# Kernel optimization log

Measured on AMD Instinct MI355X. Metric: run time of the kernel, lower is better.

Reference implementation:

```python
import jax, jax.numpy as jnp
import numpy as np

B, T, D, HS = 4, 4096, 1024, 64


def setup_inputs() -> dict:
    key = jax.random.key(0)
    k1, k2, k3 = jax.random.split(key, 3)
    x = jax.random.normal(k1, (B, T, D), dtype=jnp.float32)
    # Linear(n_embd, head_size, bias=False) weights: [head_size, n_embd]
    Wk = jax.random.normal(k2, (HS, D), dtype=jnp.float32) * (D ** -0.5)
    Wv = jax.random.normal(k3, (HS, D), dtype=jnp.float32) * (D ** -0.5)
    return {"x": x, "Wk": Wk, "Wv": Wv}


def reference(x, Wk, Wv):
    # Faithful to source: q = self.value(x) (query proj is dead code), so q and v
    # share the value projection.
    k = jnp.einsum('btd,hd->bth', x, Wk)   # [B,T,HS]
    qv = jnp.einsum('btd,hd->bth', x, Wv)  # [B,T,HS]; serves as both q and v
    scale = k.shape[-1] ** -0.5
    scores = jnp.einsum('bth,bsh->bts', qv, k) * scale  # [B,T,T]
    causal = jnp.tril(jnp.ones((T, T), dtype=bool))
    scores = jnp.where(causal, scores, -jnp.inf)
    weights = jax.nn.softmax(scores, axis=-1)
    out = jnp.einsum('bts,bsh->bth', weights, qv)  # [B,T,HS]
    return out
```

## Files before the change

### kernel.cpp

```cpp
#include <hip/hip_runtime.h>
#include <hip/hip_bf16.h>

typedef __bf16 bf16;
typedef __attribute__((ext_vector_type(4))) __bf16 bf16x4;
typedef __attribute__((ext_vector_type(8))) __bf16 bf16x8;
typedef __attribute__((ext_vector_type(4))) float f32x4;

#define T_SEQ 4096
#define D_EMB 1024
#define HS 64

__device__ __forceinline__ float fexp2(float x) {
#if __has_builtin(__builtin_amdgcn_exp2f)
    return __builtin_amdgcn_exp2f(x);
#else
    return exp2f(x);
#endif
}

__global__ __launch_bounds__(256) void wcast_kernel(
    const float* __restrict__ Wk, const float* __restrict__ Wv,
    bf16* __restrict__ wbf)
{
    const int t = blockIdx.x * 256 + threadIdx.x;
    const int base = t * 8;
    const float* src = (base < 65536) ? (Wk + base) : (Wv + base - 65536);
    float4 f0 = *(const float4*)(src);
    float4 f1 = *(const float4*)(src + 4);
    bf16x8 o = {(__bf16)f0.x, (__bf16)f0.y, (__bf16)f0.z, (__bf16)f0.w,
                (__bf16)f1.x, (__bf16)f1.y, (__bf16)f1.z, (__bf16)f1.w};
    *(bf16x8*)(wbf + base) = o;
}

__global__ __launch_bounds__(256, 2) void proj_kernel(
    const float* __restrict__ x,
    const bf16* __restrict__ wbf,
    bf16* __restrict__ kmat,
    bf16* __restrict__ qvmat,
    bf16* __restrict__ qvT)
{
    __shared__ bf16 xs[2][64][72];
    __shared__ bf16 ws[2][128][72];

    const int tid  = threadIdx.x;
    const int lane = tid & 63;
    const int wave = tid >> 6;
    const int col  = lane & 15;
    const int quad = lane >> 4;
    const int rowbase = blockIdx.x * 64;

    f32x4 acc[4][2];
#pragma unroll
    for (int mt = 0; mt < 4; ++mt)
#pragma unroll
        for (int nt = 0; nt < 2; ++nt) acc[mt][nt] = {0.f, 0.f, 0.f, 0.f};

    {
#pragma unroll
        for (int p = 0; p < 4; ++p) {
            const int idx = p * 256 + tid;
            const int xr  = idx >> 4;
            const int c4  = (idx & 15) * 4;
            float4 f = *(const float4*)(x + (size_t)(rowbase + xr) * D_EMB + c4);
            bf16x4 v = {(__bf16)f.x, (__bf16)f.y, (__bf16)f.z, (__bf16)f.w};
            *(bf16x4*)&xs[0][xr][c4] = v;
        }
#pragma unroll
        for (int p = 0; p < 4; ++p) {
            const int idx = p * 256 + tid;
            const int wr  = idx >> 3;
            const int off = (idx & 7) * 8;
            *(bf16x8*)&ws[0][wr][off] = *(const bf16x8*)(wbf + (size_t)wr * D_EMB + off);
        }
    }
    __syncthreads();

    int buf = 0;
#pragma unroll 1
    for (int c = 0; c < 16; ++c) {
        const bool more = (c + 1 < 16);

        float4 xn[4];
        bf16x8 wn[4];
        if (more) {
            const int k0 = (c + 1) * 64;
#pragma unroll
            for (int p = 0; p < 4; ++p) {
                const int idx = p * 256 + tid;
                const int xr  = idx >> 4;
                const int c4  = (idx & 15) * 4;
                xn[p] = *(const float4*)(x + (size_t)(rowbase + xr) * D_EMB + k0 + c4);
            }
#pragma unroll
            for (int p = 0; p < 4; ++p) {
                const int idx = p * 256 + tid;
                const int wr  = idx >> 3;
                const int off = (idx & 7) * 8;
                wn[p] = *(const bf16x8*)(wbf + (size_t)wr * D_EMB + k0 + off);
            }
        }

#pragma unroll
        for (int s = 0; s < 2; ++s) {
            bf16x8 af[4];
#pragma unroll
            for (int mt = 0; mt < 4; ++mt)
                af[mt] = *(const bf16x8*)&xs[buf][mt * 16 + col][s * 32 + quad * 8];
            bf16x8 bfr[2];
#pragma unroll
            for (int nt = 0; nt < 2; ++nt)
                bfr[nt] = *(const bf16x8*)&ws[buf][wave * 32 + nt * 16 + col][s * 32 + quad * 8];
#pragma unroll
            for (int mt = 0; mt < 4; ++mt)
#pragma unroll
                for (int nt = 0; nt < 2; ++nt)
                    acc[mt][nt] = __builtin_amdgcn_mfma_f32_16x16x32_bf16(
                        af[mt], bfr[nt], acc[mt][nt], 0, 0, 0);
        }

        if (more) {
#pragma unroll
            for (int p = 0; p < 4; ++p) {
                const int idx = p * 256 + tid;
                const int xr  = idx >> 4;
                const int c4  = (idx & 15) * 4;
                bf16x4 v = {(__bf16)xn[p].x, (__bf16)xn[p].y,
                            (__bf16)xn[p].z, (__bf16)xn[p].w};
                *(bf16x4*)&xs[buf ^ 1][xr][c4] = v;
            }
#pragma unroll
            for (int p = 0; p < 4; ++p) {
                const int idx = p * 256 + tid;
                const int wr  = idx >> 3;
                const int off = (idx & 7) * 8;
                *(bf16x8*)&ws[buf ^ 1][wr][off] = wn[p];
            }
            __syncthreads();
            buf ^= 1;
        }
    }

#pragma unroll
    for (int mt = 0; mt < 4; ++mt)
#pragma unroll
        for (int nt = 0; nt < 2; ++nt) {
            const int gcol = wave * 32 + nt * 16 + col;
#pragma unroll
            for (int r = 0; r < 4; ++r) {
                const int grow = rowbase + mt * 16 + quad * 4 + r;
                bf16 bv = (bf16)acc[mt][nt][r];
                if (gcol < 64) {
                    kmat[(size_t)grow * HS + gcol] = bv;
                } else {
                    const int h = gcol - 64;
                    qvmat[(size_t)grow * HS + h] = bv;
                    const int bb = grow >> 12;
                    const int tt = grow & (T_SEQ - 1);
                    qvT[((size_t)bb * HS + h) * T_SEQ + tt] = bv;
                }
            }
        }
}

__global__ __launch_bounds__(256, 3) void attn_kernel(
    const bf16* __restrict__ kmat,
    const bf16* __restrict__ qvmat,
    const bf16* __restrict__ qvT,
    float* __restrict__ out,
    float* __restrict__ o_parts,
    float* __restrict__ l_parts)
{
    __shared__ bf16 Kt[2][64][72];
    __shared__ bf16 Vt[2][64][72];
    __shared__ bf16 plds[4][16][40];

    const int tid  = threadIdx.x;
    const int lane = tid & 63;
    const int wave = tid >> 6;
    const int col  = lane & 15;
    const int quad = lane >> 4;

    const int b = blockIdx.x / 288;
    const int r = blockIdx.x - b * 288;
    int a = 0;
    while (4 * (a + 1) * (a + 2) <= r) ++a;
    const int rr = r - 4 * a * (a + 1);
    const int m  = rr / (a + 1);
    const int jc = rr - m * (a + 1);
    const int qb = 8 * a + m;

    const int cbeg  = jc * 8;
    const int nctot = qb + 1;
    const int cend  = (nctot < cbeg + 8) ? nctot : cbeg + 8;

    const bf16* qvb = qvmat + (size_t)b * T_SEQ * HS;
    const bf16* kb  = kmat  + (size_t)b * T_SEQ * HS;
    const bf16* vTb = qvT   + (size_t)b * HS * T_SEQ;

    const int q0 = qb * 64 + wave * 16;

    bf16x8 qf0 = *(const bf16x8*)(qvb + (size_t)(q0 + col) * HS + quad * 8);
    bf16x8 qf1 = *(const bf16x8*)(qvb + (size_t)(q0 + col) * HS + 32 + quad * 8);

    f32x4 o[4];
    float lp[4];
#pragma unroll
    for (int h = 0; h < 4; ++h) o[h] = {0.f, 0.f, 0.f, 0.f};
#pragma unroll
    for (int i = 0; i < 4; ++i) lp[i] = 0.f;

    const float sc = 0.125f * 1.44269504088896f;

    {
        const int kc = cbeg * 64;
#pragma unroll
        for (int it = 0; it < 2; ++it) {
            const int idx = it * 256 + tid;
            const int kr  = idx >> 3;
            const int off = (idx & 7) * 8;
            bf16x8 kv = *(const bf16x8*)(kb + (size_t)kc * HS + idx * 8);
            bf16x8 vv = *(const bf16x8*)(vTb + (size_t)kr * T_SEQ + kc + off);
            *(bf16x8*)&Kt[0][kr][off] = kv;
            *(bf16x8*)&Vt[0][kr][off] = vv;
        }
    }
    __syncthreads();

    int buf = 0;
#pragma unroll 1
    for (int c = cbeg; c < cend; ++c) {
        const bool more = (c + 1 < cend);

        bf16x8 kn[2], vn[2];
        if (more) {
            const int kcn = (c + 1) * 64;
#pragma unroll
            for (int it = 0; it < 2; ++it) {
                const int idx = it * 256 + tid;
                const int kr  = idx >> 3;
                const int off = (idx & 7) * 8;
                kn[it] = *(const bf16x8*)(kb + (size_t)kcn * HS + idx * 8);
                vn[it] = *(const bf16x8*)(vTb + (size_t)kr * T_SEQ + kcn + off);
            }
        }

        const int kc = c * 64;
#pragma unroll
        for (int st = 0; st < 2; ++st) {
            const int gk = kc + 32 * st;
            if (gk > q0 + 15) break;

            bf16x8 b0 = *(const bf16x8*)&Kt[buf][32 * st + col][quad * 8];
            bf16x8 b1 = *(const bf16x8*)&Kt[buf][32 * st + col][32 + quad * 8];
            bf16x8 b2 = *(const bf16x8*)&Kt[buf][32 * st + 16 + col][quad * 8];
            bf16x8 b3 = *(const bf16x8*)&Kt[buf][32 * st + 16 + col][32 + quad * 8];

            float p[2][4];
            {
                f32x4 a4 = {0.f, 0.f, 0.f, 0.f};
                a4 = __builtin_amdgcn_mfma_f32_16x16x32_bf16(qf0, b0, a4, 0, 0, 0);
                a4 = __builtin_amdgcn_mfma_f32_16x16x32_bf16(qf1, b1, a4, 0, 0, 0);
#pragma unroll
                for (int i = 0; i < 4; ++i) p[0][i] = fexp2(fmaf(a4[i], sc, -24.f));
            }
            {
                f32x4 a4 = {0.f, 0.f, 0.f, 0.f};
                a4 = __builtin_amdgcn_mfma_f32_16x16x32_bf16(qf0, b2, a4, 0, 0, 0);
                a4 = __builtin_amdgcn_mfma_f32_16x16x32_bf16(qf1, b3, a4, 0, 0, 0);
#pragma unroll
                for (int i = 0; i < 4; ++i) p[1][i] = fexp2(fmaf(a4[i], sc, -24.f));
            }

            if (gk + 31 > q0) {
#pragma unroll
                for (int nt = 0; nt < 2; ++nt)
#pragma unroll
                    for (int i = 0; i < 4; ++i)
                        if (gk + nt * 16 + col > q0 + quad * 4 + i)
                            p[nt][i] = 0.f;
            }

#pragma unroll
            for (int i = 0; i < 4; ++i) lp[i] += p[0][i] + p[1][i];

#pragma unroll
            for (int nt = 0; nt < 2; ++nt)
#pragma unroll
                for (int i = 0; i < 4; ++i)
                    plds[wave][quad * 4 + i][nt * 16 + col] = (bf16)p[nt][i];
            bf16x8 pa = *(const bf16x8*)&plds[wave][col][quad * 8];

#pragma unroll
            for (int h = 0; h < 4; ++h) {
                bf16x8 vb = *(const bf16x8*)&Vt[buf][h * 16 + col][32 * st + quad * 8];
                o[h] = __builtin_amdgcn_mfma_f32_16x16x32_bf16(pa, vb, o[h], 0, 0, 0);
            }
        }

        if (more) {
#pragma unroll
            for (int it = 0; it < 2; ++it) {
                const int idx = it * 256 + tid;
                const int kr  = idx >> 3;
                const int off = (idx & 7) * 8;
                *(bf16x8*)&Kt[buf ^ 1][kr][off] = kn[it];
                *(bf16x8*)&Vt[buf ^ 1][kr][off] = vn[it];
            }
            __syncthreads();
            buf ^= 1;
        }
    }

    float lr[4];
#pragma unroll
    for (int i = 0; i < 4; ++i) {
        float v = lp[i];
#pragma unroll
        for (int off = 1; off < 16; off <<= 1)
            v += __shfl_xor(v, off, 64);
        lr[i] = v;
    }

    const size_t rowbase = (size_t)b * T_SEQ + q0 + quad * 4;
    if (col == 0) {
#pragma unroll
        for (int i = 0; i < 4; ++i)
            l_parts[(size_t)jc * 16384 + rowbase + i] = lr[i];
    }

    float* dst = (jc == 0) ? out : (o_parts + (size_t)(jc - 1) * 16384 * HS);
#pragma unroll
    for (int h = 0; h < 4; ++h)
#pragma unroll
        for (int i = 0; i < 4; ++i)
            dst[(rowbase + i) * HS + h * 16 + col] = o[h][i];
}

__global__ __launch_bounds__(256) void norm_kernel(
    float* __restrict__ out,
    const float* __restrict__ o_parts,
    const float* __restrict__ l_parts)
{
    const int i   = blockIdx.x * 256 + threadIdx.x;
    const int row = i >> 6;
    const int qb  = (row & 4095) >> 6;
    const int nj  = (qb >> 3) + 1;

    float s = out[i];
    float L = l_parts[row];
    for (int j = 1; j < nj; ++j) {
        s += o_parts[(size_t)(j - 1) * 1048576 + i];
        L += l_parts[(size_t)j * 16384 + row];
    }
    out[i] = s / L;
}

extern "C" void kernel_launch(void* const* d_in, const int* in_sizes, int n_in,
                              void* d_out, int out_size, void* d_ws, size_t ws_size,
                              hipStream_t stream) {
    const float* x  = (const float*)d_in[0];
    const float* Wk = (const float*)d_in[1];
    const float* Wv = (const float*)d_in[2];
    float* out = (float*)d_out;

    bf16* ws    = (bf16*)d_ws;
    bf16* wbf   = ws;
    bf16* kmat  = ws + (size_t)128 * 1024;
    bf16* qvmat = kmat + (size_t)16384 * 64;
    bf16* qvT   = qvmat + (size_t)16384 * 64;
    float* o_parts = (float*)(qvT + (size_t)16384 * 64);
    float* l_parts = o_parts + (size_t)7 * 16384 * 64;

    wcast_kernel<<<64, 256, 0, stream>>>(Wk, Wv, wbf);
    proj_kernel<<<256, 256, 0, stream>>>(x, wbf, kmat, qvmat, qvT);
    attn_kernel<<<1152, 256, 0, stream>>>(kmat, qvmat, qvT, out, o_parts, l_parts);
    norm_kernel<<<4096, 256, 0, stream>>>(out, o_parts, l_parts);
}
```

Measured before the change: 151.2 us.

## Split projection over K with partial-sum combine; single-buffer attention LDS for occupancy

```diff
diff --git a/kernel.cpp b/kernel.cpp
--- a/kernel.cpp
+++ b/kernel.cpp
@@ -32,60 +32,74 @@
     *(bf16x8*)(wbf + base) = o;
 }
 
-__global__ __launch_bounds__(256, 2) void proj_kernel(
+__global__ __launch_bounds__(256, 4) void proj_kernel(
     const float* __restrict__ x,
     const bf16* __restrict__ wbf,
-    bf16* __restrict__ kmat,
-    bf16* __restrict__ qvmat,
-    bf16* __restrict__ qvT)
-{
-    __shared__ bf16 xs[2][64][72];
-    __shared__ bf16 ws[2][128][72];
+    float* __restrict__ pbuf)
+{
+    __shared__ bf16 xs[32][72];
+    __shared__ bf16 wsh[128][72];
 
     const int tid  = threadIdx.x;
     const int lane = tid & 63;
     const int wave = tid >> 6;
     const int col  = lane & 15;
     const int quad = lane >> 4;
-    const int rowbase = blockIdx.x * 64;
-
-    f32x4 acc[4][2];
-#pragma unroll
-    for (int mt = 0; mt < 4; ++mt)
+
+    const int mb = blockIdx.x & 511;
+    const int kh = blockIdx.x >> 9;
+    const int rowbase = mb * 32;
+    const int kbase   = kh * 512;
+
+    f32x4 acc[2][2];
+#pragma unroll
+    for (int mt = 0; mt < 2; ++mt)
 #pragma unroll
         for (int nt = 0; nt < 2; ++nt) acc[mt][nt] = {0.f, 0.f, 0.f, 0.f};
 
+    float4 xn[2];
+    bf16x8 wn[4];
     {
 #pragma unroll
-        for (int p = 0; p < 4; ++p) {
+        for (int p = 0; p < 2; ++p) {
             const int idx = p * 256 + tid;
             const int xr  = idx >> 4;
             const int c4  = (idx & 15) * 4;
-            float4 f = *(const float4*)(x + (size_t)(rowbase + xr) * D_EMB + c4);
-            bf16x4 v = {(__bf16)f.x, (__bf16)f.y, (__bf16)f.z, (__bf16)f.w};
-            *(bf16x4*)&xs[0][xr][c4] = v;
+            xn[p] = *(const float4*)(x + (size_t)(rowbase + xr) * D_EMB + kbase + c4);
         }
 #pragma unroll
         for (int p = 0; p < 4; ++p) {
             const int idx = p * 256 + tid;
             const int wr  = idx >> 3;
             const int off = (idx & 7) * 8;
-            *(bf16x8*)&ws[0][wr][off] = *(const bf16x8*)(wbf + (size_t)wr * D_EMB + off);
-        }
-    }
-    __syncthreads();
-
-    int buf = 0;
+            wn[p] = *(const bf16x8*)(wbf + (size_t)wr * D_EMB + kbase + off);
+        }
+    }
+
 #pragma unroll 1
-    for (int c = 0; c < 16; ++c) {
-        const bool more = (c + 1 < 16);
-
-        float4 xn[4];
-        bf16x8 wn[4];
-        if (more) {
-            const int k0 = (c + 1) * 64;
-#pragma unroll
-            for (int p = 0; p < 4; ++p) {
+    for (int c = 0; c < 8; ++c) {
+#pragma unroll
+        for (int p = 0; p < 2; ++p) {
+            const int idx = p * 256 + tid;
+            const int xr  = idx >> 4;
+            const int c4  = (idx & 15) * 4;
+            bf16x4 v = {(__bf16)xn[p].x, (__bf16)xn[p].y,
+                        (__bf16)xn[p].z, (__bf16)xn[p].w};
+            *(bf16x4*)&xs[xr][c4] = v;
+        }
+#pragma unroll
+        for (int p = 0; p < 4; ++p) {
+            const int idx = p * 256 + tid;
+            const int wr  = idx >> 3;
+            const int off = (idx & 7) * 8;
+            *(bf16x8*)&wsh[wr][off] = wn[p];
+        }
+        __syncthreads();
+
+        if (c < 7) {
+            const int k0 = kbase + (c + 1) * 64;
+#pragma unroll
+            for (int p = 0; p < 2; ++p) {
                 const int idx = p * 256 + tid;
                 const int xr  = idx >> 4;
                 const int c4  = (idx & 15) * 4;
@@ -102,67 +116,71 @@
 
 #pragma unroll
         for (int s = 0; s < 2; ++s) {
-            bf16x8 af[4];
-#pragma unroll
-            for (int mt = 0; mt < 4; ++mt)
-                af[mt] = *(const bf16x8*)&xs[buf][mt * 16 + col][s * 32 + quad * 8];
+            bf16x8 af[2];
+#pragma unroll
+            for (int mt = 0; mt < 2; ++mt)
+                af[mt] = *(const bf16x8*)&xs[mt * 16 + col][s * 32 + quad * 8];
             bf16x8 bfr[2];
 #pragma unroll
             for (int nt = 0; nt < 2; ++nt)
-                bfr[nt] = *(const bf16x8*)&ws[buf][wave * 32 + nt * 16 + col][s * 32 + quad * 8];
-#pragma unroll
-            for (int mt = 0; mt < 4; ++mt)
+                bfr[nt] = *(const bf16x8*)&wsh[wave * 32 + nt * 16 + col][s * 32 + quad * 8];
+#pragma unroll
+            for (int mt = 0; mt < 2; ++mt)
 #pragma unroll
                 for (int nt = 0; nt < 2; ++nt)
                     acc[mt][nt] = __builtin_amdgcn_mfma_f32_16x16x32_bf16(
                         af[mt], bfr[nt], acc[mt][nt], 0, 0, 0);
         }
-
-        if (more) {
-#pragma unroll
-            for (int p = 0; p < 4; ++p) {
-                const int idx = p * 256 + tid;
-                const int xr  = idx >> 4;
-                const int c4  = (idx & 15) * 4;
-                bf16x4 v = {(__bf16)xn[p].x, (__bf16)xn[p].y,
-                            (__bf16)xn[p].z, (__bf16)xn[p].w};
-                *(bf16x4*)&xs[buf ^ 1][xr][c4] = v;
-            }
-#pragma unroll
-            for (int p = 0; p < 4; ++p) {
-                const int idx = p * 256 + tid;
-                const int wr  = idx >> 3;
-                const int off = (idx & 7) * 8;
-                *(bf16x8*)&ws[buf ^ 1][wr][off] = wn[p];
-            }
-            __syncthreads();
-            buf ^= 1;
-        }
-    }
-
-#pragma unroll
-    for (int mt = 0; mt < 4; ++mt)
+        __syncthreads();
+    }
+
+    float* ph = pbuf + (size_t)kh * 16384 * 128;
+#pragma unroll
+    for (int mt = 0; mt < 2; ++mt)
 #pragma unroll
         for (int nt = 0; nt < 2; ++nt) {
             const int gcol = wave * 32 + nt * 16 + col;
 #pragma unroll
             for (int r = 0; r < 4; ++r) {
                 const int grow = rowbase + mt * 16 + quad * 4 + r;
-                bf16 bv = (bf16)acc[mt][nt][r];
-                if (gcol < 64) {
-                    kmat[(size_t)grow * HS + gcol] = bv;
-                } else {
-                    const int h = gcol - 64;
-                    qvmat[(size_t)grow * HS + h] = bv;
-                    const int bb = grow >> 12;
-                    const int tt = grow & (T_SEQ - 1);
-                    qvT[((size_t)bb * HS + h) * T_SEQ + tt] = bv;
-                }
-            }
-        }
-}
-
-__global__ __launch_bounds__(256, 3) void attn_kernel(
+                ph[(size_t)grow * 128 + gcol] = acc[mt][nt][r];
+            }
+        }
+}
+
+__global__ __launch_bounds__(256) void pcomb_kernel(
+    const float* __restrict__ pbuf,
+    bf16* __restrict__ kmat,
+    bf16* __restrict__ qvmat,
+    bf16* __restrict__ qvT)
+{
+    const int g   = blockIdx.x * 256 + threadIdx.x;
+    const int row = g >> 4;
+    const int cg  = g & 15;
+    const size_t base = (size_t)row * 128 + cg * 8;
+
+    f32x4 a0 = *(const f32x4*)(pbuf + base);
+    f32x4 a1 = *(const f32x4*)(pbuf + base + 4);
+    f32x4 b0 = *(const f32x4*)(pbuf + (size_t)16384 * 128 + base);
+    f32x4 b1 = *(const f32x4*)(pbuf + (size_t)16384 * 128 + base + 4);
+    a0 += b0; a1 += b1;
+    bf16x8 v = {(__bf16)a0[0], (__bf16)a0[1], (__bf16)a0[2], (__bf16)a0[3],
+                (__bf16)a1[0], (__bf16)a1[1], (__bf16)a1[2], (__bf16)a1[3]};
+
+    if (cg < 8) {
+        *(bf16x8*)(kmat + (size_t)row * HS + cg * 8) = v;
+    } else {
+        const int h0 = (cg - 8) * 8;
+        *(bf16x8*)(qvmat + (size_t)row * HS + h0) = v;
+        const int bb = row >> 12;
+        const int tt = row & (T_SEQ - 1);
+#pragma unroll
+        for (int j = 0; j < 8; ++j)
+            qvT[((size_t)bb * HS + h0 + j) * T_SEQ + tt] = v[j];
+    }
+}
+
+__global__ __launch_bounds__(256, 5) void attn_kernel(
     const bf16* __restrict__ kmat,
     const bf16* __restrict__ qvmat,
     const bf16* __restrict__ qvT,
@@ -170,8 +188,8 @@
     float* __restrict__ o_parts,
     float* __restrict__ l_parts)
 {
-    __shared__ bf16 Kt[2][64][72];
-    __shared__ bf16 Vt[2][64][72];
+    __shared__ bf16 Kt[64][72];
+    __shared__ bf16 Vt[64][72];
     __shared__ bf16 plds[4][16][40];
 
     const int tid  = threadIdx.x;
@@ -181,7 +199,7 @@
     const int quad = lane >> 4;
 
     const int b = blockIdx.x / 288;
-    const int r = blockIdx.x - b * 288;
+    const int r = 287 - (blockIdx.x - b * 288);
     int a = 0;
     while (4 * (a + 1) * (a + 2) <= r) ++a;
     const int rr = r - 4 * a * (a + 1);
@@ -211,6 +229,7 @@
 
     const float sc = 0.125f * 1.44269504088896f;
 
+    bf16x8 kn[2], vn[2];
     {
         const int kc = cbeg * 64;
 #pragma unroll
@@ -218,21 +237,24 @@
             const int idx = it * 256 + tid;
             const int kr  = idx >> 3;
             const int off = (idx & 7) * 8;
-            bf16x8 kv = *(const bf16x8*)(kb + (size_t)kc * HS + idx * 8);
-            bf16x8 vv = *(const bf16x8*)(vTb + (size_t)kr * T_SEQ + kc + off);
-            *(bf16x8*)&Kt[0][kr][off] = kv;
-            *(bf16x8*)&Vt[0][kr][off] = vv;
-        }
-    }
-    __syncthreads();
-
-    int buf = 0;
+            kn[it] = *(const bf16x8*)(kb + (size_t)kc * HS + idx * 8);
+            vn[it] = *(const bf16x8*)(vTb + (size_t)kr * T_SEQ + kc + off);
+        }
+    }
+
 #pragma unroll 1
     for (int c = cbeg; c < cend; ++c) {
-        const bool more = (c + 1 < cend);
-
-        bf16x8 kn[2], vn[2];
-        if (more) {
+#pragma unroll
+        for (int it = 0; it < 2; ++it) {
+            const int idx = it * 256 + tid;
+            const int kr  = idx >> 3;
+            const int off = (idx & 7) * 8;
+            *(bf16x8*)&Kt[kr][off] = kn[it];
+            *(bf16x8*)&Vt[kr][off] = vn[it];
+        }
+        __syncthreads();
+
+        if (c + 1 < cend) {
             const int kcn = (c + 1) * 64;
 #pragma unroll
             for (int it = 0; it < 2; ++it) {
@@ -250,10 +272,10 @@
             const int gk = kc + 32 * st;
             if (gk > q0 + 15) break;
 
-            bf16x8 b0 = *(const bf16x8*)&Kt[buf][32 * st + col][quad * 8];
-            bf16x8 b1 = *(const bf16x8*)&Kt[buf][32 * st + col][32 + quad * 8];
-            bf16x8 b2 = *(const bf16x8*)&Kt[buf][32 * st + 16 + col][quad * 8];
-            bf16x8 b3 = *(const bf16x8*)&Kt[buf][32 * st + 16 + col][32 + quad * 8];
+            bf16x8 b0 = *(const bf16x8*)&Kt[32 * st + col][quad * 8];
+            bf16x8 b1 = *(const bf16x8*)&Kt[32 * st + col][32 + quad * 8];
+            bf16x8 b2 = *(const bf16x8*)&Kt[32 * st + 16 + col][quad * 8];
+            bf16x8 b3 = *(const bf16x8*)&Kt[32 * st + 16 + col][32 + quad * 8];
 
             float p[2][4];
             {
@@ -292,23 +314,11 @@
 
 #pragma unroll
             for (int h = 0; h < 4; ++h) {
-                bf16x8 vb = *(const bf16x8*)&Vt[buf][h * 16 + col][32 * st + quad * 8];
+                bf16x8 vb = *(const bf16x8*)&Vt[h * 16 + col][32 * st + quad * 8];
                 o[h] = __builtin_amdgcn_mfma_f32_16x16x32_bf16(pa, vb, o[h], 0, 0, 0);
             }
         }
-
-        if (more) {
-#pragma unroll
-            for (int it = 0; it < 2; ++it) {
-                const int idx = it * 256 + tid;
-                const int kr  = idx >> 3;
-                const int off = (idx & 7) * 8;
-                *(bf16x8*)&Kt[buf ^ 1][kr][off] = kn[it];
-                *(bf16x8*)&Vt[buf ^ 1][kr][off] = vn[it];
-            }
-            __syncthreads();
-            buf ^= 1;
-        }
+        __syncthreads();
     }
 
     float lr[4];
@@ -370,9 +380,11 @@
     bf16* qvT   = qvmat + (size_t)16384 * 64;
     float* o_parts = (float*)(qvT + (size_t)16384 * 64);
     float* l_parts = o_parts + (size_t)7 * 16384 * 64;
+    float* pbuf    = l_parts + (size_t)8 * 16384;
 
     wcast_kernel<<<64, 256, 0, stream>>>(Wk, Wv, wbf);
-    proj_kernel<<<256, 256, 0, stream>>>(x, wbf, kmat, qvmat, qvT);
+    proj_kernel<<<1024, 256, 0, stream>>>(x, wbf, pbuf);
+    pcomb_kernel<<<1024, 256, 0, stream>>>(pbuf, kmat, qvmat, qvT);
     attn_kernel<<<1152, 256, 0, stream>>>(kmat, qvmat, qvT, out, o_parts, l_parts);
     norm_kernel<<<4096, 256, 0, stream>>>(out, o_parts, l_parts);
 }
```

Measured after the change: 147.2 us. 1.03x faster.
